# Kernel optimization log

Hardware: AMD Instinct MI355X
Metric: run time of the kernel (lower is better)

Reference implementation:

```python
import jax, jax.numpy as jnp
import numpy as np

SR = 44100        # sample rate (init arg)
WIN = 442         # FFT window length from tensor[i:i+442]
HOP = 4           # loop stride
NBINS = 221       # kept spectrum bins x[:221]
THR = 0.01        # threshold passed to inner fftLayer
REL = 0.0594      # relative pitch-change threshold
BIN_HZ = 100.0    # argmax*100 -> frequency


def _windows_and_mag(tensor):
    n = tensor.shape[0]
    n_win = (n - WIN + HOP - 1) // HOP
    starts = jnp.arange(n_win) * HOP
    windows = tensor[starts[:, None] + jnp.arange(WIN)[None, :]]
    spec = jnp.fft.fft(windows, axis=-1)[:, :NBINS]           # complex64 [n_win, 221]
    spec = jnp.where(jnp.abs(spec) < THR, jnp.zeros_like(spec), spec)  # fftLayer threshold
    mag = jnp.abs(spec.real) + jnp.abs(spec.imag)             # |re| + |im|, as in forward
    return mag, starts


def setup_inputs() -> dict:
    key = jax.random.key(0)
    return {"tensor": jax.random.normal(key, (1_000_000,), dtype=jnp.float32)}


def reference(tensor):
    mag, starts = _windows_and_mag(tensor)
    # per-window dominant frequency: argmax bin * 100 Hz
    tmp = jnp.argmax(mag, axis=-1).astype(jnp.float32) * BIN_HZ    # [n_win]
    i_samp = starts.astype(jnp.float32)                            # sample index of each window

    def step(carry, x):
        maxF, Ftime = carry
        t, i = x
        cond = jnp.abs(maxF - t) > maxF * REL
        emit_f = maxF
        emit_d = (i - Ftime) * 1000.0 / SR
        maxF = jnp.where(cond, t, maxF)
        Ftime = jnp.where(cond, i, Ftime)
        return (maxF, Ftime), (cond, emit_f, emit_d)

    (maxF, Ftime), (flags, freqs, durs) = jax.lax.scan(
        step, (jnp.float32(0.0), jnp.float32(0.0)), (tmp, i_samp))
    # trailing append after the loop: (maxF, (i_last - Ftime)*1000/44100)
    final = jnp.stack([maxF, (i_samp[-1] - Ftime) * 1000.0 / SR])
    # flags marks windows where a note boundary was emitted; (freqs, durs) at those
    # positions are the (maxF, duration_ms) pairs the original appends to `out`.
    return flags, freqs, durs, final
```

## Files before the change

### kernel.cpp

```cpp
#include <hip/hip_runtime.h>

#define WIN 442
#define HOP 4
#define NBINS 221
#define LC 128
#define SPAN 960
#define GSZ 32

constexpr double kPI = 3.14159265358979323846264338327950288;

constexpr double tsin_poly(double r) {
    double t = r, s = r;
    for (int n = 1; n <= 9; ++n) { t *= -(r * r) / ((2.0 * n) * (2.0 * n + 1.0)); s += t; }
    return s;
}
constexpr double tcos_poly(double r) {
    double t = 1.0, c = 1.0;
    for (int n = 1; n <= 9; ++n) { t *= -(r * r) / ((2.0 * n - 1.0) * (2.0 * n)); c += t; }
    return c;
}
struct SC { double s, c; };
constexpr SC tsincos(double a) {
    int q = (int)(a / (kPI / 2) + 0.5);
    double r = a - q * (kPI / 2);
    double sr = tsin_poly(r), cr = tcos_poly(r);
    switch (q & 3) {
        case 0: return {sr, cr};
        case 1: return {cr, -sr};
        case 2: return {-sr, -cr};
        default: return {-cr, sr};
    }
}
struct TabF { float c[WIN]; float s[WIN]; };
constexpr TabF make_tabf() {
    TabF t{};
    for (int i = 0; i < WIN; ++i) {
        SC sc = tsincos(2.0 * kPI * (double)i / 442.0);
        t.c[i] = (float)sc.c; t.s[i] = (float)(-sc.s);
    }
    return t;
}
struct TabR { double c4[NBINS], s4[NBINS], c8[NBINS], s8[NBINS]; };
constexpr TabR make_tabr() {
    TabR t{};
    for (int k = 0; k < NBINS; ++k) {
        SC a = tsincos(2.0 * kPI * (double)((4 * k) % WIN) / 442.0);
        t.c4[k] = a.c; t.s4[k] = a.s;
        SC b = tsincos(2.0 * kPI * (double)((8 * k) % WIN) / 442.0);
        t.c8[k] = b.c; t.s8[k] = b.s;
    }
    return t;
}
__constant__ TabF cTabF = make_tabf();
__constant__ TabR cTabR = make_tabr();

static __device__ __forceinline__ unsigned long long shflx64(unsigned long long v, int off) {
    unsigned int lo = (unsigned int)v, hi = (unsigned int)(v >> 32);
    lo = __shfl_xor(lo, off, 64);
    hi = __shfl_xor(hi, off, 64);
    return ((unsigned long long)hi << 32) | lo;
}

__global__ __launch_bounds__(128) void k_slide(
    const float* __restrict__ x, int n, int n_win, int n_chunks,
    int* __restrict__ a_arr, unsigned short* __restrict__ M0) {
    __shared__ __align__(16) float Xs[SPAN];
    __shared__ __align__(16) float Ds_[LC * 4];
    __shared__ unsigned long long cand[LC][9];

    const int tid = threadIdx.x;
    const int lane = tid & 63;
    const int wc = tid >> 6;
    const int chunk = blockIdx.x;
    const int s0 = chunk * (LC * HOP);

    for (int i = tid; i < SPAN; i += 128) {
        int g = s0 + i;
        Xs[i] = (g < n) ? x[g] : 0.0f;
    }
    __syncthreads();
    for (int r = tid; r < LC * 4; r += 128) Ds_[r] = Xs[r + WIN] - Xs[r];
    __syncthreads();

    const int wlen = min(LC, n_win - chunk * LC);

    const int k0 = lane + 128 * wc, k1 = k0 + 64;
    const bool a0 = (k0 < NBINS), a1 = (k1 < NBINS);
    const int kk0 = a0 ? k0 : 0, kk1 = a1 ? k1 : 0;
    const unsigned int lo0 = 255u - (unsigned)k0, lo1 = 255u - (unsigned)k1;

    float ec0[8], es0[8], ec1[8], es1[8];
    {
        int t0 = 0, t1 = 0;
#pragma unroll
        for (int m = 1; m < 8; ++m) {
            t0 += kk0; if (t0 >= WIN) t0 -= WIN;
            ec0[m] = cTabF.c[t0]; es0[m] = cTabF.s[t0];
            t1 += kk1; if (t1 >= WIN) t1 -= WIN;
            ec1[m] = cTabF.c[t1]; es1[m] = cTabF.s[t1];
        }
    }
    double C40 = a0 ? cTabR.c4[kk0] : 0.0, S40 = a0 ? cTabR.s4[kk0] : 0.0;
    double C41 = a1 ? cTabR.c4[kk1] : 0.0, S41 = a1 ? cTabR.s4[kk1] : 0.0;
    const double C80 = cTabR.c8[kk0], S80 = cTabR.s8[kk0];
    const double C81 = cTabR.c8[kk1], S81 = cTabR.s8[kk1];

    double S0r, S0i, S1r, S1i;
    {
        float xa = Xs[440], xb = Xs[441];
        S0r = (double)fmaf(xb, ec0[1], xa);
        S0i = (double)(xb * es0[1]);
        S1r = (double)fmaf(xb, ec1[1], xa);
        S1i = (double)(xb * es1[1]);
        const float4* Xq = (const float4*)Xs;
#pragma unroll 1
        for (int t = 54; t >= 0; --t) {
            float4 va = Xq[2 * t], vb = Xq[2 * t + 1];
            float Dr0 = va.x;
            Dr0 = fmaf(va.y, ec0[1], Dr0); Dr0 = fmaf(va.z, ec0[2], Dr0);
            Dr0 = fmaf(va.w, ec0[3], Dr0); Dr0 = fmaf(vb.x, ec0[4], Dr0);
            Dr0 = fmaf(vb.y, ec0[5], Dr0); Dr0 = fmaf(vb.z, ec0[6], Dr0);
            Dr0 = fmaf(vb.w, ec0[7], Dr0);
            float Di0 = va.y * es0[1];
            Di0 = fmaf(va.z, es0[2], Di0); Di0 = fmaf(va.w, es0[3], Di0);
            Di0 = fmaf(vb.x, es0[4], Di0); Di0 = fmaf(vb.y, es0[5], Di0);
            Di0 = fmaf(vb.z, es0[6], Di0); Di0 = fmaf(vb.w, es0[7], Di0);
            double nr = fma(S0r, C80, fma(S0i, S80, (double)Dr0));
            double ni = fma(S0i, C80, fma(S0r, -S80, (double)Di0));
            S0r = nr; S0i = ni;
            float Dr1 = va.x;
            Dr1 = fmaf(va.y, ec1[1], Dr1); Dr1 = fmaf(va.z, ec1[2], Dr1);
            Dr1 = fmaf(va.w, ec1[3], Dr1); Dr1 = fmaf(vb.x, ec1[4], Dr1);
            Dr1 = fmaf(vb.y, ec1[5], Dr1); Dr1 = fmaf(vb.z, ec1[6], Dr1);
            Dr1 = fmaf(vb.w, ec1[7], Dr1);
            float Di1 = va.y * es1[1];
            Di1 = fmaf(va.z, es1[2], Di1); Di1 = fmaf(va.w, es1[3], Di1);
            Di1 = fmaf(vb.x, es1[4], Di1); Di1 = fmaf(vb.y, es1[5], Di1);
            Di1 = fmaf(vb.z, es1[6], Di1); Di1 = fmaf(vb.w, es1[7], Di1);
            nr = fma(S1r, C81, fma(S1i, S81, (double)Dr1));
            ni = fma(S1i, C81, fma(S1r, -S81, (double)Di1));
            S1r = nr; S1i = ni;
        }
    }
    if (!a0) { S0r = 0.0; S0i = 0.0; }
    if (!a1) { S1r = 0.0; S1i = 0.0; }

    const float4* Dq = (const float4*)Ds_;
    for (int b = 0; b < 16; ++b) {
        unsigned long long key[8];
#pragma unroll
        for (int u = 0; u < 8; ++u) {
            if (b | u) {
                float4 d = Dq[b * 8 + u - 1];
                float Dr0 = fmaf(d.w, ec0[3], fmaf(d.z, ec0[2], fmaf(d.y, ec0[1], d.x)));
                float Di0 = fmaf(d.w, es0[3], fmaf(d.z, es0[2], d.y * es0[1]));
                double nr = S0r + (double)Dr0;
                double ni = S0i + (double)Di0;
                S0r = fma(nr, C40, -(ni * S40));
                S0i = fma(nr, S40, ni * C40);
                float Dr1 = fmaf(d.w, ec1[3], fmaf(d.z, ec1[2], fmaf(d.y, ec1[1], d.x)));
                float Di1 = fmaf(d.w, es1[3], fmaf(d.z, es1[2], d.y * es1[1]));
                nr = S1r + (double)Dr1;
                ni = S1i + (double)Di1;
                S1r = fma(nr, C41, -(ni * S41));
                S1i = fma(nr, S41, ni * C41);
            }
            float m0 = (float)(fabs(S0r) + fabs(S0i));
            float m1 = (float)(fabs(S1r) + fabs(S1i));
            unsigned long long key0 = ((unsigned long long)__float_as_uint(m0) << 32) | lo0;
            unsigned long long key1 = ((unsigned long long)__float_as_uint(m1) << 32) | lo1;
            key[u] = (key1 > key0) ? key1 : key0;
        }
#pragma unroll
        for (int s = 0; s < 4; ++s) {
            const int off = 32 >> s;
#pragma unroll
            for (int u = 0; u < 8; ++u) {
                unsigned long long o = shflx64(key[u], off);
                if (o > key[u]) key[u] = o;
            }
        }
        if (lane < 4) {
#pragma unroll
            for (int u = 0; u < 8; ++u) cand[b * 8 + u][wc * 4 + lane] = key[u];
        }
    }
    __syncthreads();
    float* tfl = Ds_;
    if (tid < wlen) {
        unsigned long long best = cand[tid][0];
#pragma unroll
        for (int i = 1; i < 8; ++i) {
            unsigned long long c = cand[tid][i];
            if (c > best) best = c;
        }
        int a = 255 - (int)(best & 255u);
        a_arr[chunk * LC + tid] = a;
        tfl[tid] = 100.0f * (float)a;
    }
    __syncthreads();
    {
        int b0 = tid, b1 = tid + 128;
        bool act1 = (b1 < NBINS);
        float mF0 = 100.0f * (float)b0;
        float mF1 = act1 ? 100.0f * (float)b1 : 100.0f;
        int rel0 = -1, rel1 = -1;
        for (int i = 0; i < wlen; ++i) {
            float t = tfl[i];
            if (fabsf(mF0 - t) > mF0 * 0.0594f) { mF0 = t; rel0 = i; }
            if (fabsf(mF1 - t) > mF1 * 0.0594f) { mF1 = t; rel1 = i; }
        }
        int bin0 = __float2int_rn(mF0 * 0.01f);
        M0[chunk * NBINS + b0] = (unsigned short)(((rel0 + 1) << 8) | bin0);
        if (act1) {
            int bin1 = __float2int_rn(mF1 * 0.01f);
            M0[chunk * NBINS + b1] = (unsigned short)(((rel1 + 1) << 8) | bin1);
        }
    }
}

__global__ __launch_bounds__(256) void k_sm1(const unsigned short* __restrict__ M0,
                                             int n_chunks, int* __restrict__ M1) {
    __shared__ unsigned short sm[GSZ * NBINS];
    int g = blockIdx.x;
    int c0 = g * GSZ;
    int cn = min(GSZ, n_chunks - c0);
    for (int i = threadIdx.x; i < cn * NBINS; i += 256) sm[i] = M0[c0 * NBINS + i];
    __syncthreads();
    int b = threadIdx.x;
    if (b < NBINS) {
        int bin = b, rw = -1;
        for (int i = 0; i < cn; ++i) {
            unsigned short mp = sm[i * NBINS + bin];
            if (mp >> 8) { rw = (c0 + i) * LC + (int)(mp >> 8) - 1; bin = mp & 255; }
        }
        M1[g * NBINS + b] = ((rw + 1) << 8) | bin;
    }
}

__global__ __launch_bounds__(256) void k_e0(const unsigned short* __restrict__ M0,
                                            const int* __restrict__ M1,
                                            int n_chunks, int ngrp,
                                            int* __restrict__ E0) {
    extern __shared__ char dyn[];
    int* m1s = (int*)dyn;
    unsigned short* m0s = (unsigned short*)(m1s + ngrp * NBINS);
    int g = blockIdx.x;
    int c0 = g * GSZ;
    int cn = min(GSZ, n_chunks - c0);
    for (int i = threadIdx.x; i < ngrp * NBINS; i += 256) m1s[i] = M1[i];
    for (int i = threadIdx.x; i < cn * NBINS; i += 256) m0s[i] = M0[c0 * NBINS + i];
    __syncthreads();
    int j = threadIdx.x;
    if (j < cn) {
        int bin = 0, rw = -1;
        for (int i = 0; i < g; ++i) {
            int mp = m1s[i * NBINS + bin];
            if (mp >> 8) { rw = (mp >> 8) - 1; bin = mp & 255; }
        }
        for (int q = 0; q < j; ++q) {
            unsigned short mp = m0s[q * NBINS + bin];
            if (mp >> 8) { rw = (c0 + q) * LC + (int)(mp >> 8) - 1; bin = mp & 255; }
        }
        E0[c0 + j] = ((rw + 1) << 8) | bin;
    }
}

__global__ __launch_bounds__(128) void k_emit(const int* __restrict__ a_arr,
    const int* __restrict__ E0, int n_win,
    float* __restrict__ flags, float* __restrict__ freqs, float* __restrict__ durs,
    float* __restrict__ out_final) {
    __shared__ float tf[LC];
    int j = blockIdx.x;
    int wbeg = j * LC;
    int cnt = n_win - wbeg; if (cnt > LC) cnt = LC;
    if (cnt <= 0) return;
    for (int i = threadIdx.x; i < cnt; i += 128) tf[i] = 100.0f * (float)a_arr[wbeg + i];
    __syncthreads();
    int t = threadIdx.x;
    if (t < cnt) {
        int st = E0[j];
        float maxF = 100.0f * (float)(st & 255);
        int rw = (st >> 8) - 1;
        float Ftime = (rw < 0) ? 0.0f : 4.0f * (float)rw;
        for (int i = 0; i < t; ++i) {
            float tv = tf[i];
            if (fabsf(maxF - tv) > maxF * 0.0594f) {
                maxF = tv; Ftime = 4.0f * (float)(wbeg + i);
            }
        }
        int w = wbeg + t;
        float tv = tf[t];
        float iw = 4.0f * (float)w;
        bool cond = fabsf(maxF - tv) > maxF * 0.0594f;
        flags[w] = cond ? 1.0f : 0.0f;
        freqs[w] = maxF;
        durs[w] = (iw - Ftime) * 1000.0f / 44100.0f;
        if (w == n_win - 1) {
            float fMax = cond ? tv : maxF;
            float fT   = cond ? iw : Ftime;
            out_final[0] = fMax;
            out_final[1] = (iw - fT) * 1000.0f / 44100.0f;
        }
    }
}

extern "C" void kernel_launch(void* const* d_in, const int* in_sizes, int n_in,
                              void* d_out, int out_size, void* d_ws, size_t ws_size,
                              hipStream_t stream) {
    const float* x = (const float*)d_in[0];
    int n = in_sizes[0];
    int n_win = (n - WIN + HOP - 1) / HOP;
    float* out = (float*)d_out;
    char* ws = (char*)d_ws;

    int n_chunks = (n_win + LC - 1) / LC;
    int ngrp = (n_chunks + GSZ - 1) / GSZ;

    int* a_arr         = (int*)(ws + 0);
    unsigned short* M0 = (unsigned short*)(ws + 1000448);
    int* M1            = (int*)(ws + 1864192);
    int* E0            = (int*)(ws + 1919232);

    size_t e0_lds = (size_t)ngrp * NBINS * 4 + (size_t)GSZ * NBINS * 2;

    k_slide<<<dim3(n_chunks), dim3(128), 0, stream>>>(x, n, n_win, n_chunks, a_arr, M0);
    k_sm1<<<dim3(ngrp), dim3(256), 0, stream>>>(M0, n_chunks, M1);
    k_e0<<<dim3(ngrp), dim3(256), e0_lds, stream>>>(M0, M1, n_chunks, ngrp, E0);
    k_emit<<<dim3(n_chunks), dim3(128), 0, stream>>>(a_arr, E0, n_win,
                                                     out, out + (size_t)n_win,
                                                     out + 2 * (size_t)n_win,
                                                     out + 3 * (size_t)n_win);
}
```

Measured before the change: 158.9 us.

## Fuse group-summary and chunk-entry kernels with inter-block flag synchronization

Merges the two small scan kernels into one launch. Each block publishes its group summary to global memory, sets a release flag, then spin-waits on the flags of earlier groups before composing its entry state. The group prefix is now computed once per block by thread 0 and broadcast through LDS instead of being recomputed by every thread. This removes one kernel launch and a serial global dependency, but relies on all ~62 blocks being co-resident for the spin-wait to be safe. The flags are reset inside the first kernel.

```diff
diff --git a/kernel.cpp b/kernel.cpp
--- a/kernel.cpp
+++ b/kernel.cpp
@@ -63,7 +63,8 @@
 
 __global__ __launch_bounds__(128) void k_slide(
     const float* __restrict__ x, int n, int n_win, int n_chunks,
-    int* __restrict__ a_arr, unsigned short* __restrict__ M0) {
+    int* __restrict__ a_arr, unsigned short* __restrict__ M0,
+    unsigned int* __restrict__ flags) {
     __shared__ __align__(16) float Xs[SPAN];
     __shared__ __align__(16) float Ds_[LC * 4];
     __shared__ unsigned long long cand[LC][9];
@@ -73,6 +74,8 @@
     const int wc = tid >> 6;
     const int chunk = blockIdx.x;
     const int s0 = chunk * (LC * HOP);
+
+    if (chunk == 0 && tid < 64) flags[tid] = 0u;
 
     for (int i = tid; i < SPAN; i += 128) {
         int g = s0 + i;
@@ -219,50 +222,57 @@
     }
 }
 
-__global__ __launch_bounds__(256) void k_sm1(const unsigned short* __restrict__ M0,
-                                             int n_chunks, int* __restrict__ M1) {
-    __shared__ unsigned short sm[GSZ * NBINS];
-    int g = blockIdx.x;
-    int c0 = g * GSZ;
-    int cn = min(GSZ, n_chunks - c0);
-    for (int i = threadIdx.x; i < cn * NBINS; i += 256) sm[i] = M0[c0 * NBINS + i];
-    __syncthreads();
-    int b = threadIdx.x;
-    if (b < NBINS) {
-        int bin = b, rw = -1;
-        for (int i = 0; i < cn; ++i) {
-            unsigned short mp = sm[i * NBINS + bin];
-            if (mp >> 8) { rw = (c0 + i) * LC + (int)(mp >> 8) - 1; bin = mp & 255; }
-        }
-        M1[g * NBINS + b] = ((rw + 1) << 8) | bin;
-    }
-}
-
-__global__ __launch_bounds__(256) void k_e0(const unsigned short* __restrict__ M0,
-                                            const int* __restrict__ M1,
-                                            int n_chunks, int ngrp,
-                                            int* __restrict__ E0) {
+__global__ __launch_bounds__(256) void k_sm1e0(
+    const unsigned short* __restrict__ M0, int n_chunks, int ngrp,
+    int* __restrict__ M1, unsigned int* __restrict__ flags, int* __restrict__ E0) {
     extern __shared__ char dyn[];
     int* m1s = (int*)dyn;
     unsigned short* m0s = (unsigned short*)(m1s + ngrp * NBINS);
-    int g = blockIdx.x;
-    int c0 = g * GSZ;
-    int cn = min(GSZ, n_chunks - c0);
-    for (int i = threadIdx.x; i < ngrp * NBINS; i += 256) m1s[i] = M1[i];
-    for (int i = threadIdx.x; i < cn * NBINS; i += 256) m0s[i] = M0[c0 * NBINS + i];
-    __syncthreads();
-    int j = threadIdx.x;
-    if (j < cn) {
+    __shared__ int sE1[2];
+    const int g = blockIdx.x;
+    const int tid = threadIdx.x;
+    const int c0 = g * GSZ;
+    const int cn = min(GSZ, n_chunks - c0);
+
+    for (int i = tid; i < cn * NBINS; i += 256) m0s[i] = M0[c0 * NBINS + i];
+    __syncthreads();
+    if (tid < NBINS) {
+        int bin = tid, rw = -1;
+        for (int i = 0; i < cn; ++i) {
+            unsigned short mp = m0s[i * NBINS + bin];
+            if (mp >> 8) { rw = (c0 + i) * LC + (int)(mp >> 8) - 1; bin = mp & 255; }
+        }
+        M1[g * NBINS + tid] = ((rw + 1) << 8) | bin;
+    }
+    __syncthreads();
+    if (tid == 0) {
+        __threadfence();
+        __hip_atomic_store(&flags[g], 1u, __ATOMIC_RELEASE, __HIP_MEMORY_SCOPE_AGENT);
+    }
+    if (tid < g) {
+        while (__hip_atomic_load(&flags[tid], __ATOMIC_ACQUIRE,
+                                 __HIP_MEMORY_SCOPE_AGENT) == 0u)
+            __builtin_amdgcn_s_sleep(1);
+    }
+    __syncthreads();
+    for (int i = tid; i < g * NBINS; i += 256) m1s[i] = M1[i];
+    __syncthreads();
+    if (tid == 0) {
         int bin = 0, rw = -1;
         for (int i = 0; i < g; ++i) {
             int mp = m1s[i * NBINS + bin];
             if (mp >> 8) { rw = (mp >> 8) - 1; bin = mp & 255; }
         }
-        for (int q = 0; q < j; ++q) {
+        sE1[0] = bin; sE1[1] = rw;
+    }
+    __syncthreads();
+    if (tid < cn) {
+        int bin = sE1[0], rw = sE1[1];
+        for (int q = 0; q < tid; ++q) {
             unsigned short mp = m0s[q * NBINS + bin];
             if (mp >> 8) { rw = (c0 + q) * LC + (int)(mp >> 8) - 1; bin = mp & 255; }
         }
-        E0[c0 + j] = ((rw + 1) << 8) | bin;
+        E0[c0 + tid] = ((rw + 1) << 8) | bin;
     }
 }
 
@@ -317,16 +327,18 @@
     int n_chunks = (n_win + LC - 1) / LC;
     int ngrp = (n_chunks + GSZ - 1) / GSZ;
 
-    int* a_arr         = (int*)(ws + 0);
-    unsigned short* M0 = (unsigned short*)(ws + 1000448);
-    int* M1            = (int*)(ws + 1864192);
-    int* E0            = (int*)(ws + 1919232);
-
-    size_t e0_lds = (size_t)ngrp * NBINS * 4 + (size_t)GSZ * NBINS * 2;
-
-    k_slide<<<dim3(n_chunks), dim3(128), 0, stream>>>(x, n, n_win, n_chunks, a_arr, M0);
-    k_sm1<<<dim3(ngrp), dim3(256), 0, stream>>>(M0, n_chunks, M1);
-    k_e0<<<dim3(ngrp), dim3(256), e0_lds, stream>>>(M0, M1, n_chunks, ngrp, E0);
+    int* a_arr          = (int*)(ws + 0);
+    unsigned short* M0  = (unsigned short*)(ws + 1000448);
+    int* M1             = (int*)(ws + 1864192);
+    int* E0             = (int*)(ws + 1919232);
+    unsigned int* flags = (unsigned int*)(ws + 1927168);
+
+    size_t de_lds = (size_t)ngrp * NBINS * 4 + (size_t)GSZ * NBINS * 2;
+
+    k_slide<<<dim3(n_chunks), dim3(128), 0, stream>>>(x, n, n_win, n_chunks,
+                                                      a_arr, M0, flags);
+    k_sm1e0<<<dim3(ngrp), dim3(256), de_lds, stream>>>(M0, n_chunks, ngrp,
+                                                       M1, flags, E0);
     k_emit<<<dim3(n_chunks), dim3(128), 0, stream>>>(a_arr, E0, n_win,
                                                      out, out + (size_t)n_win,
                                                      out + 2 * (size_t)n_win,
```

Result: no change. 161.5 us (+1.7%).
